# Kernel tuning notes

Hardware: AMD Instinct MI355X
Metric: run time of the kernel (lower is better)

Reference implementation:

```python
import jax, jax.numpy as jnp
import numpy as np

D = 1024
NHEAD = 16
HEAD_DIM = D // NHEAD


def setup_inputs() -> dict:
    key = jax.random.key(0)
    ks = jax.random.split(key, 7)
    B, L = 4, 2048
    q = jax.random.normal(ks[0], (B, L, D), dtype=jnp.float32)
    k = jax.random.normal(ks[1], (B, L, D), dtype=jnp.float32)
    v = jax.random.normal(ks[2], (B, L, D), dtype=jnp.float32)
    # packed QKV projection, as in nn.MultiheadAttention (in_proj_weight: [3d, d])
    scale = 1.0 / np.sqrt(D)
    in_proj_w = jax.random.uniform(ks[3], (3 * D, D), dtype=jnp.float32, minval=-scale, maxval=scale)
    in_proj_b = jnp.zeros((3 * D,), dtype=jnp.float32)
    out_w = jax.random.uniform(ks[4], (D, D), dtype=jnp.float32, minval=-scale, maxval=scale)
    out_b = jnp.zeros((D,), dtype=jnp.float32)
    return {"q": q, "k": k, "v": v, "in_proj_w": in_proj_w, "in_proj_b": in_proj_b,
            "out_w": out_w, "out_b": out_b}


def reference(q, k, v, in_proj_w, in_proj_b, out_w, out_b):
    # FP32 MHA, need_weights=True (average over heads), eval mode (dropout inactive).
    B, Lq, d = q.shape
    Lk = k.shape[1]
    # packed in-projection: rows [0:d] -> Q, [d:2d] -> K, [2d:3d] -> V
    qp = q @ in_proj_w[:d].T + in_proj_b[:d]
    kp = k @ in_proj_w[d:2 * d].T + in_proj_b[d:2 * d]
    vp = v @ in_proj_w[2 * d:].T + in_proj_b[2 * d:]
    # split heads: [B, H, L, hd]
    qp = qp.reshape(B, Lq, NHEAD, HEAD_DIM).transpose(0, 2, 1, 3)
    kp = kp.reshape(B, Lk, NHEAD, HEAD_DIM).transpose(0, 2, 1, 3)
    vp = vp.reshape(B, Lk, NHEAD, HEAD_DIM).transpose(0, 2, 1, 3)
    scores = jnp.einsum('bhqd,bhkd->bhqk', qp, kp) / jnp.sqrt(jnp.float32(HEAD_DIM))
    attn = jax.nn.softmax(scores, axis=-1)          # [B, H, Lq, Lk]
    ctx = jnp.einsum('bhqk,bhkd->bhqd', attn, vp)    # [B, H, Lq, hd]
    ctx = ctx.transpose(0, 2, 1, 3).reshape(B, Lq, d)
    out = ctx @ out_w.T + out_b                      # [B, Lq, d]
    weights = attn.mean(axis=1)                      # average over heads -> [B, Lq, Lk]
    return out, weights
```

## Files before the change

### kernel.cpp

```cpp
#include <hip/hip_runtime.h>
#include <hip/hip_bf16.h>

#define D_ 1024
#define NH 16
#define HD 64
#define B_ 4
#define L_ 2048
#define N_ (B_*L_)
#define BH_ (B_*NH)
#define QSCALE_ 0.18033688011112042f

typedef __bf16 bf16_t;
typedef __bf16 bf16x4 __attribute__((ext_vector_type(4)));
typedef __bf16 bf16x8 __attribute__((ext_vector_type(8)));
typedef float f32x4 __attribute__((ext_vector_type(4)));

typedef const __attribute__((address_space(1))) char gas_t;
typedef __attribute__((address_space(3))) char las_t;

__device__ __forceinline__ f32x4 mfma_bf16(bf16x8 a, bf16x8 b, f32x4 c) {
    return __builtin_amdgcn_mfma_f32_16x16x32_bf16(a, b, c, 0, 0, 0);
}

__device__ __forceinline__ bf16x8 cvt8_f32(const float* __restrict__ p) {
    const float4* p4 = reinterpret_cast<const float4*>(p);
    float4 a = p4[0], b = p4[1];
    bf16x8 r;
    r[0] = (bf16_t)a.x; r[1] = (bf16_t)a.y; r[2] = (bf16_t)a.z; r[3] = (bf16_t)a.w;
    r[4] = (bf16_t)b.x; r[5] = (bf16_t)b.y; r[6] = (bf16_t)b.z; r[7] = (bf16_t)b.w;
    return r;
}

__device__ __forceinline__ bf16x8 ld8_bf16(const bf16_t* __restrict__ p) {
    return *reinterpret_cast<const bf16x8*>(p);
}

__global__ __launch_bounds__(256) void k_cvt_all(
    const float* __restrict__ s0, const float* __restrict__ s1,
    const float* __restrict__ s2, const float* __restrict__ sw,
    const float* __restrict__ so,
    bf16_t* __restrict__ d0, bf16_t* __restrict__ d1, bf16_t* __restrict__ d2,
    bf16_t* __restrict__ dw, bf16_t* __restrict__ dow)
{
    const int n8  = N_ * D_ / 8;
    const int n8w = 3 * D_ * D_ / 8;
    const int n8o = D_ * D_ / 8;
    const int tot = 3 * n8 + n8w + n8o;
    int i = blockIdx.x * blockDim.x + threadIdx.x;
    int stride = gridDim.x * blockDim.x;
    for (; i < tot; i += stride) {
        const float* s; bf16_t* d; int off;
        if (i < 3 * n8) {
            int seg = i >> 20; off = i & (n8 - 1);
            s = (seg == 0) ? s0 : ((seg == 1) ? s1 : s2);
            d = (seg == 0) ? d0 : ((seg == 1) ? d1 : d2);
        } else if (i < 3 * n8 + n8w) {
            off = i - 3 * n8; s = sw; d = dw;
        } else {
            off = i - 3 * n8 - n8w; s = so; d = dow;
        }
        *reinterpret_cast<bf16x8*>(d + (size_t)off * 8) = cvt8_f32(s + (size_t)off * 8);
    }
}

__global__ __launch_bounds__(256, 4) void k_gemm_qkv(
    const bf16_t* __restrict__ qb, const bf16_t* __restrict__ kb,
    const bf16_t* __restrict__ vb, const bf16_t* __restrict__ wb,
    const float* __restrict__ bias,
    bf16_t* __restrict__ qp, bf16_t* __restrict__ kp, bf16_t* __restrict__ vpT)
{
    __shared__ __align__(16) char ldsA[2][8192];
    __shared__ __align__(16) char ldsB[2][8192];
    int tid  = threadIdx.x;
    int lane = tid & 63, w = tid >> 6;
    int r = lane & 15, g = lane >> 4;
    int wr = w >> 1, wc = w & 1;

    int bid   = blockIdx.x;
    int xcd   = bid & 7;
    int seq   = bid >> 3;
    int sec   = seq >> 6;
    int inner = seq & 63;
    int tm  = xcd * 8 + (inner >> 3);
    int ctl = (inner & 7) * 128;

    const bf16_t* A = (sec == 0) ? qb : ((sec == 1) ? kb : vb);
    const bf16_t* Ab = A + (size_t)tm * 128 * 1024;
    const bf16_t* Bb = wb + (size_t)sec * D_ * D_ + (size_t)ctl * 1024;

    f32x4 z = {0.f, 0.f, 0.f, 0.f};
    f32x4 acc[4][4];
    #pragma unroll
    for (int m = 0; m < 4; ++m)
        #pragma unroll
        for (int n = 0; n < 4; ++n) acc[m][n] = z;

    auto stage = [&](int buf, int k0) {
        #pragma unroll
        for (int i = 0; i < 2; ++i) {
            int idx = i * 256 + tid;
            int row = idx >> 2;
            int lc  = (idx & 3) ^ ((row >> 1) & 3);
            const bf16_t* gA = Ab + (size_t)row * 1024 + k0 + lc * 8;
            const bf16_t* gB = Bb + (size_t)row * 1024 + k0 + lc * 8;
            __builtin_amdgcn_global_load_lds((gas_t*)gA,
                (las_t*)(&ldsA[buf][0] + idx * 16), 16, 0, 0);
            __builtin_amdgcn_global_load_lds((gas_t*)gB,
                (las_t*)(&ldsB[buf][0] + idx * 16), 16, 0, 0);
        }
    };

    stage(0, 0);
    stage(1, 32);
    int buf = 0;

    for (int k0 = 0; k0 < 1024; k0 += 32) {
        if (k0 < 992) asm volatile("s_waitcnt vmcnt(4)" ::: "memory");
        else          asm volatile("s_waitcnt vmcnt(0)" ::: "memory");
        __builtin_amdgcn_s_barrier();
        __builtin_amdgcn_sched_barrier(0);

        bf16x8 af[4], bf_[4];
        #pragma unroll
        for (int m = 0; m < 4; ++m) {
            int R = wr * 64 + m * 16 + r;
            af[m] = *reinterpret_cast<const bf16x8*>(
                &ldsA[buf][0] + R * 64 + (((g ^ ((R >> 1) & 3)) << 4)));
        }
        #pragma unroll
        for (int n = 0; n < 4; ++n) {
            int R = wc * 64 + n * 16 + r;
            bf_[n] = *reinterpret_cast<const bf16x8*>(
                &ldsB[buf][0] + R * 64 + (((g ^ ((R >> 1) & 3)) << 4)));
        }
        #pragma unroll
        for (int m = 0; m < 4; ++m)
            #pragma unroll
            for (int n = 0; n < 4; ++n)
                acc[m][n] = mfma_bf16(af[m], bf_[n], acc[m][n]);

        __builtin_amdgcn_s_barrier();
        if (k0 + 64 < 1024) stage(buf, k0 + 64);
        buf ^= 1;
    }

    #pragma unroll
    for (int m = 0; m < 4; ++m)
        #pragma unroll
        for (int n = 0; n < 4; ++n)
            #pragma unroll
            for (int i = 0; i < 4; ++i) {
                int row = tm * 128 + wr * 64 + m * 16 + g * 4 + i;
                int col = ctl + wc * 64 + n * 16 + r;
                float val = acc[m][n][i] + bias[sec * 1024 + col];
                int bb = row >> 11, ln = row & 2047;
                int h = col >> 6, dd = col & 63;
                if (sec == 0)
                    qp[(((size_t)(bb * NH + h)) * L_ + ln) * HD + dd] =
                        (bf16_t)(val * QSCALE_);
                else if (sec == 1)
                    kp[(((size_t)(bb * NH + h)) * L_ + ln) * HD + dd] = (bf16_t)val;
                else
                    vpT[(((size_t)(bb * NH + h)) * HD + dd) * L_ + ln] = (bf16_t)val;
            }
}

__global__ __launch_bounds__(256, 4) void k_gemm_out(
    const bf16_t* __restrict__ A, const bf16_t* __restrict__ Bm,
    const float* __restrict__ bias, float* __restrict__ dst)
{
    __shared__ __align__(16) char ldsA[2][8192];
    __shared__ __align__(16) char ldsB[2][8192];
    int tid  = threadIdx.x;
    int lane = tid & 63, w = tid >> 6;
    int r = lane & 15, g = lane >> 4;
    int wr = w >> 1, wc = w & 1;

    int bid = blockIdx.x;
    int swz = (bid & 7) * 64 + (bid >> 3);
    int tm = swz >> 3, tn = swz & 7;

    const bf16_t* Ab = A  + (size_t)tm * 128 * 1024;
    const bf16_t* Bb = Bm + (size_t)tn * 128 * 1024;

    f32x4 z = {0.f, 0.f, 0.f, 0.f};
    f32x4 acc[4][4];
    #pragma unroll
    for (int m = 0; m < 4; ++m)
        #pragma unroll
        for (int n = 0; n < 4; ++n) acc[m][n] = z;

    auto stage = [&](int buf, int k0) {
        #pragma unroll
        for (int i = 0; i < 2; ++i) {
            int idx = i * 256 + tid;
            int row = idx >> 2;
            int lc  = (idx & 3) ^ ((row >> 1) & 3);
            const bf16_t* gA = Ab + (size_t)row * 1024 + k0 + lc * 8;
            const bf16_t* gB = Bb + (size_t)row * 1024 + k0 + lc * 8;
            __builtin_amdgcn_global_load_lds((gas_t*)gA,
                (las_t*)(&ldsA[buf][0] + idx * 16), 16, 0, 0);
            __builtin_amdgcn_global_load_lds((gas_t*)gB,
                (las_t*)(&ldsB[buf][0] + idx * 16), 16, 0, 0);
        }
    };

    stage(0, 0);
    stage(1, 32);
    int buf = 0;

    for (int k0 = 0; k0 < 1024; k0 += 32) {
        if (k0 < 992) asm volatile("s_waitcnt vmcnt(4)" ::: "memory");
        else          asm volatile("s_waitcnt vmcnt(0)" ::: "memory");
        __builtin_amdgcn_s_barrier();
        __builtin_amdgcn_sched_barrier(0);

        bf16x8 af[4], bf_[4];
        #pragma unroll
        for (int m = 0; m < 4; ++m) {
            int R = wr * 64 + m * 16 + r;
            af[m] = *reinterpret_cast<const bf16x8*>(
                &ldsA[buf][0] + R * 64 + (((g ^ ((R >> 1) & 3)) << 4)));
        }
        #pragma unroll
        for (int n = 0; n < 4; ++n) {
            int R = wc * 64 + n * 16 + r;
            bf_[n] = *reinterpret_cast<const bf16x8*>(
                &ldsB[buf][0] + R * 64 + (((g ^ ((R >> 1) & 3)) << 4)));
        }
        #pragma unroll
        for (int m = 0; m < 4; ++m)
            #pragma unroll
            for (int n = 0; n < 4; ++n)
                acc[m][n] = mfma_bf16(af[m], bf_[n], acc[m][n]);

        __builtin_amdgcn_s_barrier();
        if (k0 + 64 < 1024) stage(buf, k0 + 64);
        buf ^= 1;
    }

    #pragma unroll
    for (int m = 0; m < 4; ++m)
        #pragma unroll
        for (int n = 0; n < 4; ++n)
            #pragma unroll
            for (int i = 0; i < 4; ++i) {
                int row = tm * 128 + wr * 64 + m * 16 + g * 4 + i;
                int col = tn * 128 + wc * 64 + n * 16 + r;
                dst[(size_t)row * 1024 + col] = acc[m][n][i] + bias[col];
            }
}

__global__ __launch_bounds__(256, 4) void k_attn(
    const bf16_t* __restrict__ qp, const bf16_t* __restrict__ kp,
    const bf16_t* __restrict__ vpT,
    bf16_t* __restrict__ ctx, float* __restrict__ lInvOut)
{
    __shared__ __align__(16) char sK[8192];
    __shared__ __align__(16) char sV[8192];
    __shared__ __align__(16) char sP[4][4096];

    int tid  = threadIdx.x;
    int w    = tid >> 6;
    int lane = tid & 63;
    int r = lane & 15, g = lane >> 4;
    int bh = blockIdx.x & 63;
    int qg = blockIdx.x >> 6;
    int qbase = qg * 128 + w * 32;

    const bf16_t* qpb = qp  + (size_t)bh * L_ * HD;
    const bf16_t* kpb = kp  + (size_t)bh * L_ * HD;
    const bf16_t* vtb = vpT + (size_t)bh * HD * L_;

    bf16x8 bq[2][2];
    #pragma unroll
    for (int qt = 0; qt < 2; ++qt)
        #pragma unroll
        for (int ds = 0; ds < 2; ++ds)
            bq[qt][ds] = ld8_bf16(qpb + (size_t)(qbase + qt * 16 + r) * HD + ds * 32 + g * 8);

    bf16x8 ones;
    #pragma unroll
    for (int i = 0; i < 8; ++i) ones[i] = (bf16_t)1.0f;

    f32x4 z = {0.f, 0.f, 0.f, 0.f};
    f32x4 acc[2][4];
    #pragma unroll
    for (int qt = 0; qt < 2; ++qt)
        #pragma unroll
        for (int dt = 0; dt < 4; ++dt) acc[qt][dt] = z;
    f32x4 acc_l[2];
    acc_l[0] = z; acc_l[1] = z;

    char* Pw = &sP[w][0];

    int srow = tid >> 3;
    int slc  = (tid & 7) ^ (srow & 7);
    const bf16_t* gK0 = kpb + (size_t)srow * HD + slc * 8;
    const bf16_t* gV0 = vtb + (size_t)srow * L_ + slc * 8;

    for (int kt = 0; kt < 32; ++kt) {
        int k0 = kt * 64;
        const bf16_t* gK = gK0 + (size_t)k0 * HD;
        const bf16_t* gV = gV0 + k0;
        #pragma unroll
        for (int i = 0; i < 2; ++i) {
            __builtin_amdgcn_global_load_lds((gas_t*)(gK + (size_t)i * 32 * HD),
                (las_t*)(&sK[0] + i * 4096 + tid * 16), 16, 0, 0);
            __builtin_amdgcn_global_load_lds((gas_t*)(gV + (size_t)i * 32 * L_),
                (las_t*)(&sV[0] + i * 4096 + tid * 16), 16, 0, 0);
        }
        __syncthreads();

        f32x4 sT[4][2];
        __builtin_amdgcn_s_setprio(1);
        #pragma unroll
        for (int ktile = 0; ktile < 4; ++ktile) {
            bf16x8 a0 = *reinterpret_cast<const bf16x8*>(
                &sK[0] + (ktile * 16 + r) * 128 + (((g    ) ^ (r & 7)) << 4));
            bf16x8 a1 = *reinterpret_cast<const bf16x8*>(
                &sK[0] + (ktile * 16 + r) * 128 + (((4 + g) ^ (r & 7)) << 4));
            #pragma unroll
            for (int qt = 0; qt < 2; ++qt) {
                f32x4 t = mfma_bf16(a0, bq[qt][0], z);
                sT[ktile][qt] = mfma_bf16(a1, bq[qt][1], t);
            }
        }
        __builtin_amdgcn_s_setprio(0);

        #pragma unroll
        for (int qt = 0; qt < 2; ++qt) {
            #pragma unroll
            for (int ktile = 0; ktile < 4; ++ktile) {
                bf16x4 pw;
                #pragma unroll
                for (int i = 0; i < 4; ++i)
                    pw[i] = (bf16_t)__builtin_amdgcn_exp2f(sT[ktile][qt][i]);
                *reinterpret_cast<bf16x4*>(Pw + (qt * 16 + r) * 128 +
                    (((2 * ktile + (g >> 1)) ^ (r & 7)) << 4) + ((g & 1) << 3)) = pw;
            }
        }

        bf16x8 pa[2][2];
        #pragma unroll
        for (int qt = 0; qt < 2; ++qt)
            #pragma unroll
            for (int ks = 0; ks < 2; ++ks)
                pa[qt][ks] = *reinterpret_cast<const bf16x8*>(
                    Pw + (qt * 16 + r) * 128 + (((4 * ks + g) ^ (r & 7)) << 4));
        __builtin_amdgcn_s_setprio(1);
        #pragma unroll
        for (int qt = 0; qt < 2; ++qt) {
            acc_l[qt] = mfma_bf16(pa[qt][0], ones, acc_l[qt]);
            acc_l[qt] = mfma_bf16(pa[qt][1], ones, acc_l[qt]);
        }
        #pragma unroll
        for (int dt = 0; dt < 4; ++dt)
            #pragma unroll
            for (int ks = 0; ks < 2; ++ks) {
                bf16x8 bv = *reinterpret_cast<const bf16x8*>(
                    &sV[0] + (dt * 16 + r) * 128 + (((4 * ks + g) ^ (r & 7)) << 4));
                acc[0][dt] = mfma_bf16(pa[0][ks], bv, acc[0][dt]);
                acc[1][dt] = mfma_bf16(pa[1][ks], bv, acc[1][dt]);
            }
        __builtin_amdgcn_s_setprio(0);

        __syncthreads();
    }

    int bb = bh >> 4, h = bh & 15;
    #pragma unroll
    for (int qt = 0; qt < 2; ++qt) {
        float lq[4];
        #pragma unroll
        for (int i = 0; i < 4; ++i) lq[i] = 1.0f / acc_l[qt][i];
        #pragma unroll
        for (int i = 0; i < 4; ++i) {
            int q = qbase + qt * 16 + 4 * g + i;
            #pragma unroll
            for (int dt = 0; dt < 4; ++dt) {
                float val = acc[qt][dt][i] * lq[i];
                ctx[(((size_t)(bb * L_ + q)) * NH + h) * HD + dt * 16 + r] = (bf16_t)val;
            }
        }
        if (r == 0) {
            #pragma unroll
            for (int i = 0; i < 4; ++i) {
                int q = qbase + qt * 16 + 4 * g + i;
                lInvOut[(size_t)bh * L_ + q] = lq[i];
            }
        }
    }
}

__global__ __launch_bounds__(256, 2) void k_weights(
    const bf16_t* __restrict__ qp, const bf16_t* __restrict__ kp,
    const float* __restrict__ lInv, float* __restrict__ wout)
{
    __shared__ __align__(16) char sQ[2][16384];
    __shared__ __align__(16) char sKt[2][16384];
    __shared__ __align__(16) float sLi[16][128];

    int tid  = threadIdx.x;
    int w    = tid >> 6;
    int lane = tid & 63;
    int r = lane & 15, g = lane >> 4;
    int wr = w >> 1, wc = w & 1;

    int wgid = (blockIdx.x & 7) * 128 + (blockIdx.x >> 3);
    int chunk = wgid >> 7;
    int b  = chunk >> 1;
    int qh = chunk & 1;
    int rem = wgid & 127;
    int qt = qh * 8 + (rem >> 4);
    int kt = rem & 15;
    int q0 = qt * 128, k0 = kt * 128;

    #pragma unroll
    for (int i = 0; i < 2; ++i) {
        int idx = i * 256 + tid;
        int h   = idx >> 5;
        int off = (idx & 31) * 4;
        const float* gl = lInv + ((size_t)(b * NH + h) * L_ + q0 + off);
        __builtin_amdgcn_global_load_lds((gas_t*)gl,
            (las_t*)((char*)&sLi[0][0] + i * 4096 + w * 1024), 16, 0, 0);
    }

    auto stage_qk = [&](int buf, int h) {
        const bf16_t* Qh = qp + ((size_t)(b * NH + h) * L_ + q0) * HD;
        const bf16_t* Kh = kp + ((size_t)(b * NH + h) * L_ + k0) * HD;
        #pragma unroll
        for (int i = 0; i < 4; ++i) {
            int idx = i * 256 + tid;
            int row = idx >> 3;
            int lc  = (idx & 7) ^ (row & 7);
            const bf16_t* gQ = Qh + (size_t)row * HD + lc * 8;
            const bf16_t* gK = Kh + (size_t)row * HD + lc * 8;
            __builtin_amdgcn_global_load_lds((gas_t*)gQ,
                (las_t*)(&sQ[buf][0]  + i * 4096 + w * 1024), 16, 0, 0);
            __builtin_amdgcn_global_load_lds((gas_t*)gK,
                (las_t*)(&sKt[buf][0] + i * 4096 + w * 1024), 16, 0, 0);
        }
    };

    float acc[4][4][4] = {};
    f32x4 z = {0.f, 0.f, 0.f, 0.f};

    stage_qk(0, 0);
    __syncthreads();
    int buf = 0;

    for (int h = 0; h < NH; ++h) {
        if (h + 1 < NH) stage_qk(buf ^ 1, h + 1);

        const char* Qb = &sQ[buf][0];
        const char* Kb = &sKt[buf][0];

        bf16x8 bfrag[4][2];
        #pragma unroll
        for (int nf = 0; nf < 4; ++nf) {
            int R = wc * 64 + nf * 16 + r;
            bfrag[nf][0] = *reinterpret_cast<const bf16x8*>(
                Kb + R * 128 + (((g    ) ^ (R & 7)) << 4));
            bfrag[nf][1] = *reinterpret_cast<const bf16x8*>(
                Kb + R * 128 + (((4 + g) ^ (R & 7)) << 4));
        }
        #pragma unroll
        for (int mf = 0; mf < 4; ++mf) {
            int R = wr * 64 + mf * 16 + r;
            bf16x8 af0 = *reinterpret_cast<const bf16x8*>(
                Qb + R * 128 + (((g    ) ^ (R & 7)) << 4));
            bf16x8 af1 = *reinterpret_cast<const bf16x8*>(
                Qb + R * 128 + (((4 + g) ^ (R & 7)) << 4));
            int qrow = wr * 64 + mf * 16 + g * 4;
            f32x4 liv = *reinterpret_cast<const f32x4*>(&sLi[h][qrow]);
            #pragma unroll
            for (int nf = 0; nf < 4; ++nf) {
                f32x4 t = mfma_bf16(af0, bfrag[nf][0], z);
                t = mfma_bf16(af1, bfrag[nf][1], t);
                #pragma unroll
                for (int i = 0; i < 4; ++i)
                    acc[mf][nf][i] += __builtin_amdgcn_exp2f(t[i]) * liv[i];
            }
        }
        __syncthreads();
        buf ^= 1;
    }

    const float inv_h = 1.0f / (float)NH;
    #pragma unroll
    for (int mf = 0; mf < 4; ++mf)
        #pragma unroll
        for (int nf = 0; nf < 4; ++nf)
            #pragma unroll
            for (int i = 0; i < 4; ++i) {
                int qidx = q0 + wr * 64 + mf * 16 + g * 4 + i;
                int kidx = k0 + wc * 64 + nf * 16 + r;
                wout[((size_t)(b * L_ + qidx)) * L_ + kidx] = acc[mf][nf][i] * inv_h;
            }
}

extern "C" void kernel_launch(void* const* d_in, const int* in_sizes, int n_in,
                              void* d_out, int out_size, void* d_ws, size_t ws_size,
                              hipStream_t stream) {
    const float* q     = (const float*)d_in[0];
    const float* k     = (const float*)d_in[1];
    const float* v     = (const float*)d_in[2];
    const float* in_w  = (const float*)d_in[3];
    const float* in_b  = (const float*)d_in[4];
    const float* out_w = (const float*)d_in[5];
    const float* out_b = (const float*)d_in[6];

    char* ws = (char*)d_ws;
    bf16_t* xb   = (bf16_t*)(ws);
    bf16_t* wb   = (bf16_t*)(ws + ((size_t)48 << 20));
    bf16_t* owb  = (bf16_t*)(ws + ((size_t)54 << 20));
    bf16_t* qp   = (bf16_t*)(ws + ((size_t)56 << 20));
    bf16_t* kp   = (bf16_t*)(ws + ((size_t)72 << 20));
    bf16_t* vpT  = (bf16_t*)(ws + ((size_t)88 << 20));
    bf16_t* ctx  = (bf16_t*)(ws + ((size_t)104 << 20));
    float*  lBuf = (float*)(ws + ((size_t)120 << 20));

    bf16_t* qb = xb;
    bf16_t* kb = xb + (size_t)N_ * D_;
    bf16_t* vb = xb + (size_t)2 * N_ * D_;

    float* outp = (float*)d_out;
    float* wout = outp + (size_t)N_ * D_;

    k_cvt_all<<<2048, 256, 0, stream>>>(q, k, v, in_w, out_w, qb, kb, vb, wb, owb);

    k_gemm_qkv<<<1536, 256, 0, stream>>>(qb, kb, vb, wb, in_b, qp, kp, vpT);

    k_attn<<<1024, 256, 0, stream>>>(qp, kp, vpT, ctx, lBuf);

    k_weights<<<1024, 256, 0, stream>>>(qp, kp, lBuf, wout);

    k_gemm_out<<<512, 256, 0, stream>>>(ctx, owb, out_b, outp);
}
```

Before: 266.8 us.

## Enlarge QKV GEMM tile to 256x128 with 512 threads and K-step 64

The QKV projection GEMM now uses 512-thread blocks computing 256x128 output tiles with a K step of 64 instead of 32, halving the grid to 768 blocks. LDS staging grows to 96 KB with an 8-way XOR swizzle, and each wave issues two MFMAs per k-slice. The aim is more reuse of B tiles across rows and fewer barrier/loop iterations per unit of work. The cost is occupancy limited to one block per CU and fewer blocks to balance across CUs.

New measurement: 267.3 us. No clear change (+0.2%).

```diff
diff --git a/kernel.cpp b/kernel.cpp
--- a/kernel.cpp
+++ b/kernel.cpp
@@ -63,29 +63,33 @@
     }
 }
 
-__global__ __launch_bounds__(256, 4) void k_gemm_qkv(
+__global__ __launch_bounds__(512, 1) void k_gemm_qkv(
     const bf16_t* __restrict__ qb, const bf16_t* __restrict__ kb,
     const bf16_t* __restrict__ vb, const bf16_t* __restrict__ wb,
     const float* __restrict__ bias,
     bf16_t* __restrict__ qp, bf16_t* __restrict__ kp, bf16_t* __restrict__ vpT)
 {
-    __shared__ __align__(16) char ldsA[2][8192];
-    __shared__ __align__(16) char ldsB[2][8192];
+    __shared__ __align__(16) char ldsA[65536];
+    __shared__ __align__(16) char ldsB[32768];
+
     int tid  = threadIdx.x;
-    int lane = tid & 63, w = tid >> 6;
+    int lane = tid & 63;
+    int wid  = tid >> 6;
     int r = lane & 15, g = lane >> 4;
-    int wr = w >> 1, wc = w & 1;
-
-    int bid   = blockIdx.x;
-    int xcd   = bid & 7;
-    int seq   = bid >> 3;
-    int sec   = seq >> 6;
-    int inner = seq & 63;
-    int tm  = xcd * 8 + (inner >> 3);
-    int ctl = (inner & 7) * 128;
+    int wr = wid >> 1;
+    int wc = wid & 1;
+
+    int bid = blockIdx.x;
+    int xcd = bid & 7;
+    int seq = bid >> 3;
+    int sec = seq >> 5;
+    int inner = seq & 31;
+    int tm  = xcd * 4 + (inner >> 3);
+    int tn  = inner & 7;
+    int ctl = tn * 128;
 
     const bf16_t* A = (sec == 0) ? qb : ((sec == 1) ? kb : vb);
-    const bf16_t* Ab = A + (size_t)tm * 128 * 1024;
+    const bf16_t* Ab = A + (size_t)tm * 256 * 1024;
     const bf16_t* Bb = wb + (size_t)sec * D_ * D_ + (size_t)ctl * 1024;
 
     f32x4 z = {0.f, 0.f, 0.f, 0.f};
@@ -95,52 +99,66 @@
         #pragma unroll
         for (int n = 0; n < 4; ++n) acc[m][n] = z;
 
-    auto stage = [&](int buf, int k0) {
-        #pragma unroll
-        for (int i = 0; i < 2; ++i) {
-            int idx = i * 256 + tid;
-            int row = idx >> 2;
-            int lc  = (idx & 3) ^ ((row >> 1) & 3);
+    auto stage = [&](int buf, int t) {
+        int k0 = t * 64;
+        #pragma unroll
+        for (int j = 0; j < 4; ++j) {
+            int idx = j * 512 + tid;
+            int row = idx >> 3;
+            int lc  = (idx & 7) ^ (row & 7);
             const bf16_t* gA = Ab + (size_t)row * 1024 + k0 + lc * 8;
+            __builtin_amdgcn_global_load_lds((gas_t*)gA,
+                (las_t*)(&ldsA[0] + buf * 32768 + idx * 16), 16, 0, 0);
+        }
+        #pragma unroll
+        for (int j = 0; j < 2; ++j) {
+            int idx = j * 512 + tid;
+            int row = idx >> 3;
+            int lc  = (idx & 7) ^ (row & 7);
             const bf16_t* gB = Bb + (size_t)row * 1024 + k0 + lc * 8;
-            __builtin_amdgcn_global_load_lds((gas_t*)gA,
-                (las_t*)(&ldsA[buf][0] + idx * 16), 16, 0, 0);
             __builtin_amdgcn_global_load_lds((gas_t*)gB,
-                (las_t*)(&ldsB[buf][0] + idx * 16), 16, 0, 0);
+                (las_t*)(&ldsB[0] + buf * 16384 + idx * 16), 16, 0, 0);
         }
     };
 
     stage(0, 0);
-    stage(1, 32);
+    stage(1, 1);
     int buf = 0;
 
-    for (int k0 = 0; k0 < 1024; k0 += 32) {
-        if (k0 < 992) asm volatile("s_waitcnt vmcnt(4)" ::: "memory");
-        else          asm volatile("s_waitcnt vmcnt(0)" ::: "memory");
+    for (int t = 0; t < 16; ++t) {
+        if (t < 15) asm volatile("s_waitcnt vmcnt(6)" ::: "memory");
+        else        asm volatile("s_waitcnt vmcnt(0)" ::: "memory");
         __builtin_amdgcn_s_barrier();
         __builtin_amdgcn_sched_barrier(0);
 
-        bf16x8 af[4], bf_[4];
+        const char* Al = &ldsA[0] + buf * 32768;
+        const char* Bl = &ldsB[0] + buf * 16384;
+
+        bf16x8 bf_[4][2];
+        #pragma unroll
+        for (int n = 0; n < 4; ++n) {
+            int R = wc * 64 + n * 16 + r;
+            bf_[n][0] = *reinterpret_cast<const bf16x8*>(
+                Bl + R * 128 + ((((g    ) ^ (R & 7)) << 4)));
+            bf_[n][1] = *reinterpret_cast<const bf16x8*>(
+                Bl + R * 128 + ((((4 + g) ^ (R & 7)) << 4)));
+        }
         #pragma unroll
         for (int m = 0; m < 4; ++m) {
             int R = wr * 64 + m * 16 + r;
-            af[m] = *reinterpret_cast<const bf16x8*>(
-                &ldsA[buf][0] + R * 64 + (((g ^ ((R >> 1) & 3)) << 4)));
-        }
-        #pragma unroll
-        for (int n = 0; n < 4; ++n) {
-            int R = wc * 64 + n * 16 + r;
-            bf_[n] = *reinterpret_cast<const bf16x8*>(
-                &ldsB[buf][0] + R * 64 + (((g ^ ((R >> 1) & 3)) << 4)));
-        }
-        #pragma unroll
-        for (int m = 0; m < 4; ++m)
-            #pragma unroll
-            for (int n = 0; n < 4; ++n)
-                acc[m][n] = mfma_bf16(af[m], bf_[n], acc[m][n]);
+            bf16x8 af0 = *reinterpret_cast<const bf16x8*>(
+                Al + R * 128 + ((((g    ) ^ (R & 7)) << 4)));
+            bf16x8 af1 = *reinterpret_cast<const bf16x8*>(
+                Al + R * 128 + ((((4 + g) ^ (R & 7)) << 4)));
+            #pragma unroll
+            for (int n = 0; n < 4; ++n) {
+                acc[m][n] = mfma_bf16(af0, bf_[n][0], acc[m][n]);
+                acc[m][n] = mfma_bf16(af1, bf_[n][1], acc[m][n]);
+            }
+        }
 
         __builtin_amdgcn_s_barrier();
-        if (k0 + 64 < 1024) stage(buf, k0 + 64);
+        if (t + 2 < 16) stage(buf, t + 2);
         buf ^= 1;
     }
 
@@ -150,7 +168,7 @@
         for (int n = 0; n < 4; ++n)
             #pragma unroll
             for (int i = 0; i < 4; ++i) {
-                int row = tm * 128 + wr * 64 + m * 16 + g * 4 + i;
+                int row = tm * 256 + wr * 64 + m * 16 + g * 4 + i;
                 int col = ctl + wc * 64 + n * 16 + r;
                 float val = acc[m][n][i] + bias[sec * 1024 + col];
                 int bb = row >> 11, ln = row & 2047;
@@ -530,7 +548,7 @@
 
     k_cvt_all<<<2048, 256, 0, stream>>>(q, k, v, in_w, out_w, qb, kb, vb, wb, owb);
 
-    k_gemm_qkv<<<1536, 256, 0, stream>>>(qb, kb, vb, wb, in_b, qp, kp, vpT);
+    k_gemm_qkv<<<768, 512, 0, stream>>>(qb, kb, vb, wb, in_b, qp, kp, vpT);
 
     k_attn<<<1024, 256, 0, stream>>>(qp, kp, vpT, ctx, lBuf);
 
```
